# Performance work log

Hardware: AMD Instinct MI355X
Metric: run time of the kernel (lower is better)

## Reference

```python
import jax, jax.numpy as jnp
import numpy as np

N_NODES = 50000
N_EDGES = 600000
DIM = 128
NUM_CLASSES = 10
EPS = 1e-15
MAX_NORM = 1.0 - 1e-5  # keep points strictly inside the unit ball for artanh


def _norm(x):
    return jnp.maximum(jnp.linalg.norm(x, axis=-1, keepdims=True), EPS)


def logmap0(x):
    # Poincare ball, c=1: artanh(||x||) * x / ||x||
    n = _norm(x)
    return jnp.arctanh(jnp.minimum(n, MAX_NORM)) * x / n


def expmap0(u):
    # Poincare ball, c=1: tanh(||u||) * u / ||u||
    n = _norm(u)
    return jnp.tanh(n) * u / n


def hyp_conv(x, W, b, src, dst):
    t = logmap0(x)                       # [N, D] manifold -> tangent at origin
    h = t @ W.T + b                      # [N, D] linear in tangent space
    y = expmap0(h)                       # [N, D] back to manifold
    # message passing: gather source features, scatter-add at destinations
    return jax.ops.segment_sum(y[src], dst, num_segments=N_NODES)


def setup_inputs() -> dict:
    key = jax.random.key(0)
    ks = jax.random.split(key, 8)
    edge_index = jax.random.randint(ks[0], (2, N_EDGES), 0, N_NODES, dtype=jnp.int64)
    # entity embeddings: small tangent vectors mapped onto the ball
    x = expmap0(0.01 * jax.random.normal(ks[1], (N_NODES, DIM), dtype=jnp.float32))
    s = 1.0 / np.sqrt(DIM)
    W1 = jax.random.normal(ks[2], (DIM, DIM), dtype=jnp.float32) * s
    b1 = jax.random.normal(ks[3], (DIM,), dtype=jnp.float32) * 0.01
    W2 = jax.random.normal(ks[4], (DIM, DIM), dtype=jnp.float32) * s
    b2 = jax.random.normal(ks[5], (DIM,), dtype=jnp.float32) * 0.01
    Wc = jax.random.normal(ks[6], (NUM_CLASSES, DIM), dtype=jnp.float32) * s
    bc = jax.random.normal(ks[7], (NUM_CLASSES,), dtype=jnp.float32) * 0.01
    return {"edge_index": edge_index, "x": x, "W1": W1, "b1": b1,
            "W2": W2, "b2": b2, "Wc": Wc, "bc": bc}


def reference(edge_index, x, W1, b1, W2, b2, Wc, bc):
    src, dst = edge_index[0], edge_index[1]
    h = hyp_conv(x, W1, b1, src, dst)
    h = jax.nn.relu(h)
    h = hyp_conv(h, W2, b2, src, dst)
    h = jax.nn.relu(h)
    t = logmap0(h)
    return t @ Wc.T + bc  # [N_NODES, NUM_CLASSES]
```

## Files before the change

### kernel.cpp

```cpp
#include <hip/hip_runtime.h>

#define N_NODES 50000
#define N_EDGES 600000
#define DIM 128
#define NCLS 10
#define ELLW 64
#define CURSTRIDE 16
#define EPSF 1e-15f
#define MAXNORM 0.99999f
#define NTILE ((N_NODES + 63) / 64)
#define FILL_BLOCKS 586
#define XFORM_BLOCKS 512

typedef __attribute__((ext_vector_type(8))) short bf16x8;
typedef __attribute__((ext_vector_type(4))) float f32x4;

__device__ inline float waveSum(float v) {
#pragma unroll
  for (int o = 1; o < 64; o <<= 1) v += __shfl_xor(v, o, 64);
  return v;
}

__device__ inline unsigned short f2bf(float f) {
  union { float f; unsigned u; } c; c.f = f;
  return (unsigned short)((c.u + 0x7FFFu + ((c.u >> 16) & 1u)) >> 16);
}
__device__ inline float bf_lo(unsigned u) {
  union { unsigned u; float f; } c; c.u = u << 16; return c.f;
}
__device__ inline float bf_hi(unsigned u) {
  union { unsigned u; float f; } c; c.u = u & 0xFFFF0000u; return c.f;
}

__global__ __launch_bounds__(256) void init_kernel(
    int* __restrict__ cursor, const float* __restrict__ W1, const float* __restrict__ W2,
    unsigned short* __restrict__ W1b, unsigned short* __restrict__ W2b)
{
  int i = blockIdx.x * 256 + threadIdx.x;
  if (i < N_NODES) cursor[i * CURSTRIDE] = 0;
  if (i < DIM * DIM) {
    W1b[i] = f2bf(W1[i]);
    W2b[i] = f2bf(W2[i]);
  }
}

__global__ __launch_bounds__(256, 2) void fill_transform(
    const int* __restrict__ src, const int* __restrict__ dst,
    int* __restrict__ cursor, int* __restrict__ ell,
    const float* __restrict__ x, const unsigned short* __restrict__ Wb,
    const float* __restrict__ b, unsigned short* __restrict__ y)
{
  __shared__ __align__(16) unsigned short At[64 * DIM];

  if (blockIdx.x < FILL_BLOCKS) {
    const int nthr = FILL_BLOCKS * 256;
    const int e = blockIdx.x * 256 + threadIdx.x;
    const int e0 = e, e1 = e + nthr, e2 = e + 2 * nthr, e3 = e + 3 * nthr;
    int d0, d1, d2, d3, s0, s1, s2, s3;
    if (e0 < N_EDGES) { d0 = dst[e0]; s0 = src[e0]; }
    if (e1 < N_EDGES) { d1 = dst[e1]; s1 = src[e1]; }
    if (e2 < N_EDGES) { d2 = dst[e2]; s2 = src[e2]; }
    if (e3 < N_EDGES) { d3 = dst[e3]; s3 = src[e3]; }
    int p0, p1, p2, p3;
    if (e0 < N_EDGES) p0 = atomicAdd(&cursor[d0 * CURSTRIDE], 1);
    if (e1 < N_EDGES) p1 = atomicAdd(&cursor[d1 * CURSTRIDE], 1);
    if (e2 < N_EDGES) p2 = atomicAdd(&cursor[d2 * CURSTRIDE], 1);
    if (e3 < N_EDGES) p3 = atomicAdd(&cursor[d3 * CURSTRIDE], 1);
    if (e0 < N_EDGES) ell[d0 * ELLW + p0] = s0;
    if (e1 < N_EDGES) ell[d1 * ELLW + p1] = s1;
    if (e2 < N_EDGES) ell[d2 * ELLW + p2] = s2;
    if (e3 < N_EDGES) ell[d3 * ELLW + p3] = s3;
    return;
  }

  const int tid = threadIdx.x;
  const int w = tid >> 6;
  const int l = tid & 63;
  const int lr = l & 15;
  const int lg = l >> 4;

  bf16x8 bf[8][4];
#pragma unroll
  for (int n = 0; n < 8; ++n)
#pragma unroll
    for (int kc = 0; kc < 4; ++kc)
      bf[n][kc] = *(const bf16x8*)(Wb + (n * 16 + lr) * DIM + kc * 32 + lg * 8);

  float bias[8];
#pragma unroll
  for (int n = 0; n < 8; ++n) bias[n] = b[n * 16 + lr];

  const int row = w * 16 + lr;

  for (int tile = blockIdx.x - FILL_BLOCKS; tile < NTILE; tile += XFORM_BLOCKS) {
    const int base = tile * 64;
    const int node = base + row;
    __syncthreads();

    float v[32];
    if (node < N_NODES) {
      const float4* xr = (const float4*)(x + (size_t)node * DIM + lg * 32);
#pragma unroll
      for (int q = 0; q < 8; ++q) {
        float4 f = xr[q];
        v[q * 4 + 0] = f.x; v[q * 4 + 1] = f.y; v[q * 4 + 2] = f.z; v[q * 4 + 3] = f.w;
      }
    } else {
#pragma unroll
      for (int q = 0; q < 32; ++q) v[q] = 0.f;
    }
    float sq = 0.f;
#pragma unroll
    for (int q = 0; q < 32; ++q) sq += v[q] * v[q];
    sq += __shfl_xor(sq, 16, 64);
    sq += __shfl_xor(sq, 32, 64);
    float n1 = sqrtf(sq);
    float nc = fmaxf(n1, EPSF);
    float nm = fminf(nc, MAXNORM);
    float scale = 0.5f * logf((1.f + nm) / (1.f - nm)) / nc;
#pragma unroll
    for (int s = 0; s < 4; ++s) {
      unsigned short tmp[8];
#pragma unroll
      for (int e = 0; e < 8; ++e) tmp[e] = f2bf(v[s * 8 + e] * scale);
      int byte = row * 256 + lg * 64 + s * 16;
      byte ^= (row & 7) << 4;
      *(bf16x8*)((char*)At + byte) = *(const bf16x8*)tmp;
    }
    __syncthreads();

    f32x4 acc[8];
#pragma unroll
    for (int n = 0; n < 8; ++n) {
      acc[n][0] = bias[n]; acc[n][1] = bias[n]; acc[n][2] = bias[n]; acc[n][3] = bias[n];
    }
#pragma unroll
    for (int kc = 0; kc < 4; ++kc) {
      int arow = w * 16 + lr;
      int byte = arow * 256 + kc * 64 + lg * 16;
      byte ^= (arow & 7) << 4;
      bf16x8 af = *(const bf16x8*)((const char*)At + byte);
#pragma unroll
      for (int n = 0; n < 8; ++n)
        acc[n] = __builtin_amdgcn_mfma_f32_16x16x32_bf16(af, bf[n][kc], acc[n], 0, 0, 0);
    }

    float rs[4];
#pragma unroll
    for (int j = 0; j < 4; ++j) {
      float s2 = 0.f;
#pragma unroll
      for (int n = 0; n < 8; ++n) s2 += acc[n][j] * acc[n][j];
      s2 += __shfl_xor(s2, 1, 64);
      s2 += __shfl_xor(s2, 2, 64);
      s2 += __shfl_xor(s2, 4, 64);
      s2 += __shfl_xor(s2, 8, 64);
      float n2 = sqrtf(s2);
      float n2c = fmaxf(n2, EPSF);
      rs[j] = tanhf(n2c) / n2c;
    }
#pragma unroll
    for (int j = 0; j < 4; ++j) {
      int nrow = base + w * 16 + lg * 4 + j;
      if (nrow < N_NODES) {
        unsigned short* yr = y + (size_t)nrow * DIM + lr;
#pragma unroll
        for (int n = 0; n < 8; ++n) yr[n * 16] = f2bf(acc[n][j] * rs[j]);
      }
    }
  }
}

__global__ __launch_bounds__(256) void gatherT_kernel(
    const unsigned short* __restrict__ y, const int* __restrict__ cursor,
    const int* __restrict__ ell, unsigned short* __restrict__ tout)
{
  const int node = blockIdx.x * 4 + (threadIdx.x >> 6);
  if (node >= N_NODES) return;
  const int lane = threadIdx.x & 63;
  const int* lst = ell + node * ELLW;
  const int cnt = cursor[node * CURSTRIDE];
  float2 a0 = {0.f, 0.f}, a1 = {0.f, 0.f}, a2 = {0.f, 0.f}, a3 = {0.f, 0.f};
  int j = 0;
  for (; j + 7 < cnt; j += 8) {
    unsigned u0 = ((const unsigned*)(y + (size_t)lst[j    ] * DIM))[lane];
    unsigned u1 = ((const unsigned*)(y + (size_t)lst[j + 1] * DIM))[lane];
    unsigned u2 = ((const unsigned*)(y + (size_t)lst[j + 2] * DIM))[lane];
    unsigned u3 = ((const unsigned*)(y + (size_t)lst[j + 3] * DIM))[lane];
    unsigned u4 = ((const unsigned*)(y + (size_t)lst[j + 4] * DIM))[lane];
    unsigned u5 = ((const unsigned*)(y + (size_t)lst[j + 5] * DIM))[lane];
    unsigned u6 = ((const unsigned*)(y + (size_t)lst[j + 6] * DIM))[lane];
    unsigned u7 = ((const unsigned*)(y + (size_t)lst[j + 7] * DIM))[lane];
    a0.x += bf_lo(u0); a0.y += bf_hi(u0);
    a1.x += bf_lo(u1); a1.y += bf_hi(u1);
    a2.x += bf_lo(u2); a2.y += bf_hi(u2);
    a3.x += bf_lo(u3); a3.y += bf_hi(u3);
    a0.x += bf_lo(u4); a0.y += bf_hi(u4);
    a1.x += bf_lo(u5); a1.y += bf_hi(u5);
    a2.x += bf_lo(u6); a2.y += bf_hi(u6);
    a3.x += bf_lo(u7); a3.y += bf_hi(u7);
  }
  for (; j + 3 < cnt; j += 4) {
    unsigned u0 = ((const unsigned*)(y + (size_t)lst[j    ] * DIM))[lane];
    unsigned u1 = ((const unsigned*)(y + (size_t)lst[j + 1] * DIM))[lane];
    unsigned u2 = ((const unsigned*)(y + (size_t)lst[j + 2] * DIM))[lane];
    unsigned u3 = ((const unsigned*)(y + (size_t)lst[j + 3] * DIM))[lane];
    a0.x += bf_lo(u0); a0.y += bf_hi(u0);
    a1.x += bf_lo(u1); a1.y += bf_hi(u1);
    a2.x += bf_lo(u2); a2.y += bf_hi(u2);
    a3.x += bf_lo(u3); a3.y += bf_hi(u3);
  }
  for (; j < cnt; ++j) {
    unsigned u0 = ((const unsigned*)(y + (size_t)lst[j] * DIM))[lane];
    a0.x += bf_lo(u0); a0.y += bf_hi(u0);
  }
  float2 r;
  r.x = fmaxf((a0.x + a1.x) + (a2.x + a3.x), 0.f);
  r.y = fmaxf((a0.y + a1.y) + (a2.y + a3.y), 0.f);

  float s = waveSum(r.x * r.x + r.y * r.y);
  float n = sqrtf(s);
  float nc = fmaxf(n, EPSF);
  float nm = fminf(nc, MAXNORM);
  float scale = 0.5f * logf((1.0f + nm) / (1.0f - nm)) / nc;
  unsigned u = (unsigned)f2bf(r.x * scale) | ((unsigned)f2bf(r.y * scale) << 16);
  ((unsigned*)(tout + (size_t)node * DIM))[lane] = u;
}

__global__ __launch_bounds__(256, 2) void transform2_mfma(
    const unsigned short* __restrict__ t, const unsigned short* __restrict__ Wb,
    const float* __restrict__ b, unsigned short* __restrict__ y)
{
  const int tid = threadIdx.x;
  const int w = tid >> 6;
  const int l = tid & 63;
  const int lr = l & 15;
  const int lg = l >> 4;

  __shared__ __align__(16) unsigned short At[64 * DIM];

  bf16x8 bf[8][4];
#pragma unroll
  for (int n = 0; n < 8; ++n)
#pragma unroll
    for (int kc = 0; kc < 4; ++kc)
      bf[n][kc] = *(const bf16x8*)(Wb + (n * 16 + lr) * DIM + kc * 32 + lg * 8);

  float bias[8];
#pragma unroll
  for (int n = 0; n < 8; ++n) bias[n] = b[n * 16 + lr];

  const int row = w * 16 + lr;

  for (int tile = blockIdx.x; tile < NTILE; tile += gridDim.x) {
    const int base = tile * 64;
    const int node = base + row;
    __syncthreads();

#pragma unroll
    for (int s = 0; s < 4; ++s) {
      bf16x8 frag;
      if (node < N_NODES)
        frag = *(const bf16x8*)(t + (size_t)node * DIM + lg * 32 + s * 8);
      else
        frag = bf16x8{0, 0, 0, 0, 0, 0, 0, 0};
      int byte = row * 256 + lg * 64 + s * 16;
      byte ^= (row & 7) << 4;
      *(bf16x8*)((char*)At + byte) = frag;
    }
    __syncthreads();

    f32x4 acc[8];
#pragma unroll
    for (int n = 0; n < 8; ++n) {
      acc[n][0] = bias[n]; acc[n][1] = bias[n]; acc[n][2] = bias[n]; acc[n][3] = bias[n];
    }
#pragma unroll
    for (int kc = 0; kc < 4; ++kc) {
      int arow = w * 16 + lr;
      int byte = arow * 256 + kc * 64 + lg * 16;
      byte ^= (arow & 7) << 4;
      bf16x8 af = *(const bf16x8*)((const char*)At + byte);
#pragma unroll
      for (int n = 0; n < 8; ++n)
        acc[n] = __builtin_amdgcn_mfma_f32_16x16x32_bf16(af, bf[n][kc], acc[n], 0, 0, 0);
    }

    float rs[4];
#pragma unroll
    for (int j = 0; j < 4; ++j) {
      float s2 = 0.f;
#pragma unroll
      for (int n = 0; n < 8; ++n) s2 += acc[n][j] * acc[n][j];
      s2 += __shfl_xor(s2, 1, 64);
      s2 += __shfl_xor(s2, 2, 64);
      s2 += __shfl_xor(s2, 4, 64);
      s2 += __shfl_xor(s2, 8, 64);
      float n2 = sqrtf(s2);
      float n2c = fmaxf(n2, EPSF);
      rs[j] = tanhf(n2c) / n2c;
    }
#pragma unroll
    for (int j = 0; j < 4; ++j) {
      int nrow = base + w * 16 + lg * 4 + j;
      if (nrow < N_NODES) {
        unsigned short* yr = y + (size_t)nrow * DIM + lr;
#pragma unroll
        for (int n = 0; n < 8; ++n) yr[n * 16] = f2bf(acc[n][j] * rs[j]);
      }
    }
  }
}

__global__ __launch_bounds__(256) void head_mfma(
    const unsigned short* __restrict__ t2, const float* __restrict__ Wc,
    const float* __restrict__ bc, float* __restrict__ out)
{
  const int base = blockIdx.x * 64;
  const int w = threadIdx.x >> 6;
  const int l = threadIdx.x & 63;
  const int lr = l & 15;
  const int lg = l >> 4;

  bf16x8 bw[4];
#pragma unroll
  for (int kc = 0; kc < 4; ++kc) {
    unsigned short tmp[8];
    if (lr < NCLS) {
      const float* wr = Wc + (size_t)lr * DIM + kc * 32 + lg * 8;
#pragma unroll
      for (int e = 0; e < 8; ++e) tmp[e] = f2bf(wr[e]);
    } else {
#pragma unroll
      for (int e = 0; e < 8; ++e) tmp[e] = 0;
    }
    bw[kc] = *(const bf16x8*)tmp;
  }
  const float bias = (lr < NCLS) ? bc[lr] : 0.f;

  const int arow = base + w * 16 + lr;
  f32x4 acc;
  acc[0] = bias; acc[1] = bias; acc[2] = bias; acc[3] = bias;
#pragma unroll
  for (int kc = 0; kc < 4; ++kc) {
    bf16x8 af;
    if (arow < N_NODES)
      af = *(const bf16x8*)(t2 + (size_t)arow * DIM + kc * 32 + lg * 8);
    else
      af = bf16x8{0, 0, 0, 0, 0, 0, 0, 0};
    acc = __builtin_amdgcn_mfma_f32_16x16x32_bf16(af, bw[kc], acc, 0, 0, 0);
  }

  if (lr < NCLS) {
#pragma unroll
    for (int j = 0; j < 4; ++j) {
      int nrow = base + w * 16 + lg * 4 + j;
      if (nrow < N_NODES) out[(size_t)nrow * NCLS + lr] = acc[j];
    }
  }
}

extern "C" void kernel_launch(void* const* d_in, const int* in_sizes, int n_in,
                              void* d_out, int out_size, void* d_ws, size_t ws_size,
                              hipStream_t stream)
{
  const int* edge = (const int*)d_in[0];
  const int* src = edge;
  const int* dst = edge + N_EDGES;
  const float* x  = (const float*)d_in[1];
  const float* W1 = (const float*)d_in[2];
  const float* b1 = (const float*)d_in[3];
  const float* W2 = (const float*)d_in[4];
  const float* b2 = (const float*)d_in[5];
  const float* Wc = (const float*)d_in[6];
  const float* bc = (const float*)d_in[7];
  float* out = (float*)d_out;

  unsigned short* ybuf = (unsigned short*)d_ws;
  unsigned short* tbuf = ybuf + (size_t)N_NODES * DIM;
  unsigned short* W1b = tbuf + (size_t)N_NODES * DIM;
  unsigned short* W2b = W1b + DIM * DIM;
  int* cursor = (int*)(W2b + DIM * DIM);
  int* ell    = cursor + (size_t)N_NODES * CURSTRIDE;

  init_kernel<<<(N_NODES + 255) / 256, 256, 0, stream>>>(cursor, W1, W2, W1b, W2b);

  fill_transform<<<FILL_BLOCKS + XFORM_BLOCKS, 256, 0, stream>>>(
      src, dst, cursor, ell, x, W1b, b1, ybuf);

  gatherT_kernel<<<(N_NODES + 3) / 4, 256, 0, stream>>>(ybuf, cursor, ell, tbuf);

  transform2_mfma<<<512, 256, 0, stream>>>(tbuf, W2b, b2, ybuf);

  gatherT_kernel<<<(N_NODES + 3) / 4, 256, 0, stream>>>(ybuf, cursor, ell, tbuf);

  head_mfma<<<NTILE, 256, 0, stream>>>(tbuf, Wc, bc, out);
}
```

Measured before the change: 135.9 us.

## Build ELL adjacency via two-pass bucketed binning with LDS-local placement

Edges are first appended, with one atomic each, into coarse buckets of 128 destination nodes split into 8 sub-cursors, storing packed (local dst, src) words. A new binfill kernel then builds each bucket's ELL tile in shared memory using LDS atomics, writes it out with coalesced int4 stores, and records per-node degrees. This replaces scattered global atomics on 50k per-node cursors and random ell writes with contended bucket atomics plus an extra pass and launch. It risks overflow if a sub-bucket exceeds CAP or a node exceeds ELLW, and the 16-bit src packing only works because node ids stay below 65536.

```diff
diff --git a/kernel.cpp b/kernel.cpp
--- a/kernel.cpp
+++ b/kernel.cpp
@@ -5,7 +5,10 @@
 #define DIM 128
 #define NCLS 10
 #define ELLW 64
-#define CURSTRIDE 16
+#define NBUCK 391
+#define SUBC 8
+#define CAP 384
+#define CPAD 16
 #define EPSF 1e-15f
 #define MAXNORM 0.99999f
 #define NTILE ((N_NODES + 63) / 64)
@@ -33,11 +36,11 @@
 }
 
 __global__ __launch_bounds__(256) void init_kernel(
-    int* __restrict__ cursor, const float* __restrict__ W1, const float* __restrict__ W2,
+    int* __restrict__ bcur, const float* __restrict__ W1, const float* __restrict__ W2,
     unsigned short* __restrict__ W1b, unsigned short* __restrict__ W2b)
 {
   int i = blockIdx.x * 256 + threadIdx.x;
-  if (i < N_NODES) cursor[i * CURSTRIDE] = 0;
+  if (i < NBUCK * SUBC * CPAD) bcur[i] = 0;
   if (i < DIM * DIM) {
     W1b[i] = f2bf(W1[i]);
     W2b[i] = f2bf(W2[i]);
@@ -46,7 +49,7 @@
 
 __global__ __launch_bounds__(256, 2) void fill_transform(
     const int* __restrict__ src, const int* __restrict__ dst,
-    int* __restrict__ cursor, int* __restrict__ ell,
+    int* __restrict__ bcur, unsigned* __restrict__ interm,
     const float* __restrict__ x, const unsigned short* __restrict__ Wb,
     const float* __restrict__ b, unsigned short* __restrict__ y)
 {
@@ -55,6 +58,7 @@
   if (blockIdx.x < FILL_BLOCKS) {
     const int nthr = FILL_BLOCKS * 256;
     const int e = blockIdx.x * 256 + threadIdx.x;
+    const int q = threadIdx.x & (SUBC - 1);
     const int e0 = e, e1 = e + nthr, e2 = e + 2 * nthr, e3 = e + 3 * nthr;
     int d0, d1, d2, d3, s0, s1, s2, s3;
     if (e0 < N_EDGES) { d0 = dst[e0]; s0 = src[e0]; }
@@ -62,14 +66,14 @@
     if (e2 < N_EDGES) { d2 = dst[e2]; s2 = src[e2]; }
     if (e3 < N_EDGES) { d3 = dst[e3]; s3 = src[e3]; }
     int p0, p1, p2, p3;
-    if (e0 < N_EDGES) p0 = atomicAdd(&cursor[d0 * CURSTRIDE], 1);
-    if (e1 < N_EDGES) p1 = atomicAdd(&cursor[d1 * CURSTRIDE], 1);
-    if (e2 < N_EDGES) p2 = atomicAdd(&cursor[d2 * CURSTRIDE], 1);
-    if (e3 < N_EDGES) p3 = atomicAdd(&cursor[d3 * CURSTRIDE], 1);
-    if (e0 < N_EDGES) ell[d0 * ELLW + p0] = s0;
-    if (e1 < N_EDGES) ell[d1 * ELLW + p1] = s1;
-    if (e2 < N_EDGES) ell[d2 * ELLW + p2] = s2;
-    if (e3 < N_EDGES) ell[d3 * ELLW + p3] = s3;
+    if (e0 < N_EDGES) p0 = atomicAdd(&bcur[((d0 >> 7) * SUBC + q) * CPAD], 1);
+    if (e1 < N_EDGES) p1 = atomicAdd(&bcur[((d1 >> 7) * SUBC + q) * CPAD], 1);
+    if (e2 < N_EDGES) p2 = atomicAdd(&bcur[((d2 >> 7) * SUBC + q) * CPAD], 1);
+    if (e3 < N_EDGES) p3 = atomicAdd(&bcur[((d3 >> 7) * SUBC + q) * CPAD], 1);
+    if (e0 < N_EDGES) interm[(size_t)((d0 >> 7) * SUBC + q) * CAP + p0] = ((unsigned)(d0 & 127) << 16) | (unsigned)s0;
+    if (e1 < N_EDGES) interm[(size_t)((d1 >> 7) * SUBC + q) * CAP + p1] = ((unsigned)(d1 & 127) << 16) | (unsigned)s1;
+    if (e2 < N_EDGES) interm[(size_t)((d2 >> 7) * SUBC + q) * CAP + p2] = ((unsigned)(d2 & 127) << 16) | (unsigned)s2;
+    if (e3 < N_EDGES) interm[(size_t)((d3 >> 7) * SUBC + q) * CAP + p3] = ((unsigned)(d3 & 127) << 16) | (unsigned)s3;
     return;
   }
 
@@ -171,15 +175,48 @@
   }
 }
 
+__global__ __launch_bounds__(256) void binfill_kernel(
+    const unsigned* __restrict__ interm, const int* __restrict__ bcur,
+    int* __restrict__ ell, int* __restrict__ deg)
+{
+  __shared__ int tile[128 * ELLW];
+  __shared__ int lcur[128];
+  const int b = blockIdx.x;
+  const int tid = threadIdx.x;
+  if (tid < 128) lcur[tid] = 0;
+  __syncthreads();
+#pragma unroll
+  for (int q = 0; q < SUBC; ++q) {
+    int c = bcur[(b * SUBC + q) * CPAD];
+    c = min(c, CAP);
+    const unsigned* seg = interm + (size_t)(b * SUBC + q) * CAP;
+    for (int i = tid; i < c; i += 256) {
+      unsigned u = seg[i];
+      int d = u >> 16, s = (int)(u & 0xFFFFu);
+      int slot = atomicAdd(&lcur[d], 1);
+      tile[d * ELLW + slot] = s;
+    }
+  }
+  __syncthreads();
+  int4* dstp = (int4*)(ell + (size_t)b * 128 * ELLW);
+  const int4* srcp = (const int4*)tile;
+#pragma unroll
+  for (int k = 0; k < 8; ++k) dstp[tid + k * 256] = srcp[tid + k * 256];
+  if (tid < 128) {
+    int node = b * 128 + tid;
+    if (node < N_NODES) deg[node] = lcur[tid];
+  }
+}
+
 __global__ __launch_bounds__(256) void gatherT_kernel(
-    const unsigned short* __restrict__ y, const int* __restrict__ cursor,
+    const unsigned short* __restrict__ y, const int* __restrict__ deg,
     const int* __restrict__ ell, unsigned short* __restrict__ tout)
 {
   const int node = blockIdx.x * 4 + (threadIdx.x >> 6);
   if (node >= N_NODES) return;
   const int lane = threadIdx.x & 63;
-  const int* lst = ell + node * ELLW;
-  const int cnt = cursor[node * CURSTRIDE];
+  const int* lst = ell + (size_t)node * ELLW;
+  const int cnt = deg[node];
   float2 a0 = {0.f, 0.f}, a1 = {0.f, 0.f}, a2 = {0.f, 0.f}, a3 = {0.f, 0.f};
   int j = 0;
   for (; j + 7 < cnt; j += 8) {
@@ -380,19 +417,23 @@
   unsigned short* tbuf = ybuf + (size_t)N_NODES * DIM;
   unsigned short* W1b = tbuf + (size_t)N_NODES * DIM;
   unsigned short* W2b = W1b + DIM * DIM;
-  int* cursor = (int*)(W2b + DIM * DIM);
-  int* ell    = cursor + (size_t)N_NODES * CURSTRIDE;
-
-  init_kernel<<<(N_NODES + 255) / 256, 256, 0, stream>>>(cursor, W1, W2, W1b, W2b);
+  int* bcur = (int*)(W2b + DIM * DIM);
+  unsigned* interm = (unsigned*)(bcur + NBUCK * SUBC * CPAD);
+  int* ell = (int*)(interm + (size_t)NBUCK * SUBC * CAP);
+  int* deg = ell + (size_t)NBUCK * 128 * ELLW;
+
+  init_kernel<<<(N_NODES + 255) / 256, 256, 0, stream>>>(bcur, W1, W2, W1b, W2b);
 
   fill_transform<<<FILL_BLOCKS + XFORM_BLOCKS, 256, 0, stream>>>(
-      src, dst, cursor, ell, x, W1b, b1, ybuf);
-
-  gatherT_kernel<<<(N_NODES + 3) / 4, 256, 0, stream>>>(ybuf, cursor, ell, tbuf);
+      src, dst, bcur, interm, x, W1b, b1, ybuf);
+
+  binfill_kernel<<<NBUCK, 256, 0, stream>>>(interm, bcur, ell, deg);
+
+  gatherT_kernel<<<(N_NODES + 3) / 4, 256, 0, stream>>>(ybuf, deg, ell, tbuf);
 
   transform2_mfma<<<512, 256, 0, stream>>>(tbuf, W2b, b2, ybuf);
 
-  gatherT_kernel<<<(N_NODES + 3) / 4, 256, 0, stream>>>(ybuf, cursor, ell, tbuf);
+  gatherT_kernel<<<(N_NODES + 3) / 4, 256, 0, stream>>>(ybuf, deg, ell, tbuf);
 
   head_mfma<<<NTILE, 256, 0, stream>>>(tbuf, Wc, bc, out);
 }
```

After: 146.7 us. 7.9% more time.

## Partition edge-bucket cursors into eight sub-lists to reduce atomic contention

Applied to the files above, without the earlier changes.

Edge bucketing now uses 8 partitions, chosen by block index, each with its own dense cursor array and a 16-slot ELL list per node, in place of one padded cursor per node. Fill runs one edge per thread across 2344 blocks. The gather kernel loops over the 8 partitions with a 2-way unrolled accumulation. The aim is to spread atomic traffic over more addresses and shrink the padded cursor footprint. The risk is silently dropping edges when a node gets more than 16 in one partition, and more cursor loads per node in the gather.

```diff
diff --git a/kernel.cpp b/kernel.cpp
--- a/kernel.cpp
+++ b/kernel.cpp
@@ -4,13 +4,13 @@
 #define N_EDGES 600000
 #define DIM 128
 #define NCLS 10
-#define ELLW 64
-#define CURSTRIDE 16
+#define NPART 8
+#define ELLW_P 16
 #define EPSF 1e-15f
 #define MAXNORM 0.99999f
 #define NTILE ((N_NODES + 63) / 64)
-#define FILL_BLOCKS 586
-#define XFORM_BLOCKS 512
+#define FILLB 2344
+#define XFB 512
 
 typedef __attribute__((ext_vector_type(8))) short bf16x8;
 typedef __attribute__((ext_vector_type(4))) float f32x4;
@@ -33,11 +33,11 @@
 }
 
 __global__ __launch_bounds__(256) void init_kernel(
-    int* __restrict__ cursor, const float* __restrict__ W1, const float* __restrict__ W2,
+    int* __restrict__ cur, const float* __restrict__ W1, const float* __restrict__ W2,
     unsigned short* __restrict__ W1b, unsigned short* __restrict__ W2b)
 {
   int i = blockIdx.x * 256 + threadIdx.x;
-  if (i < N_NODES) cursor[i * CURSTRIDE] = 0;
+  if (i < NPART * N_NODES) cur[i] = 0;
   if (i < DIM * DIM) {
     W1b[i] = f2bf(W1[i]);
     W2b[i] = f2bf(W2[i]);
@@ -46,30 +46,21 @@
 
 __global__ __launch_bounds__(256, 2) void fill_transform(
     const int* __restrict__ src, const int* __restrict__ dst,
-    int* __restrict__ cursor, int* __restrict__ ell,
+    int* __restrict__ cur, int* __restrict__ ell,
     const float* __restrict__ x, const unsigned short* __restrict__ Wb,
     const float* __restrict__ b, unsigned short* __restrict__ y)
 {
   __shared__ __align__(16) unsigned short At[64 * DIM];
 
-  if (blockIdx.x < FILL_BLOCKS) {
-    const int nthr = FILL_BLOCKS * 256;
+  if (blockIdx.x < FILLB) {
     const int e = blockIdx.x * 256 + threadIdx.x;
-    const int e0 = e, e1 = e + nthr, e2 = e + 2 * nthr, e3 = e + 3 * nthr;
-    int d0, d1, d2, d3, s0, s1, s2, s3;
-    if (e0 < N_EDGES) { d0 = dst[e0]; s0 = src[e0]; }
-    if (e1 < N_EDGES) { d1 = dst[e1]; s1 = src[e1]; }
-    if (e2 < N_EDGES) { d2 = dst[e2]; s2 = src[e2]; }
-    if (e3 < N_EDGES) { d3 = dst[e3]; s3 = src[e3]; }
-    int p0, p1, p2, p3;
-    if (e0 < N_EDGES) p0 = atomicAdd(&cursor[d0 * CURSTRIDE], 1);
-    if (e1 < N_EDGES) p1 = atomicAdd(&cursor[d1 * CURSTRIDE], 1);
-    if (e2 < N_EDGES) p2 = atomicAdd(&cursor[d2 * CURSTRIDE], 1);
-    if (e3 < N_EDGES) p3 = atomicAdd(&cursor[d3 * CURSTRIDE], 1);
-    if (e0 < N_EDGES) ell[d0 * ELLW + p0] = s0;
-    if (e1 < N_EDGES) ell[d1 * ELLW + p1] = s1;
-    if (e2 < N_EDGES) ell[d2 * ELLW + p2] = s2;
-    if (e3 < N_EDGES) ell[d3 * ELLW + p3] = s3;
+    if (e < N_EDGES) {
+      const int part = blockIdx.x & (NPART - 1);
+      int d = dst[e];
+      int s = src[e];
+      int p = atomicAdd(&cur[part * N_NODES + d], 1);
+      if (p < ELLW_P) ell[((size_t)part * N_NODES + d) * ELLW_P + p] = s;
+    }
     return;
   }
 
@@ -92,7 +83,7 @@
 
   const int row = w * 16 + lr;
 
-  for (int tile = blockIdx.x - FILL_BLOCKS; tile < NTILE; tile += XFORM_BLOCKS) {
+  for (int tile = blockIdx.x - FILLB; tile < NTILE; tile += XFB) {
     const int base = tile * 64;
     const int node = base + row;
     __syncthreads();
@@ -136,9 +127,8 @@
     }
 #pragma unroll
     for (int kc = 0; kc < 4; ++kc) {
-      int arow = w * 16 + lr;
-      int byte = arow * 256 + kc * 64 + lg * 16;
-      byte ^= (arow & 7) << 4;
+      int byte = row * 256 + kc * 64 + lg * 16;
+      byte ^= (row & 7) << 4;
       bf16x8 af = *(const bf16x8*)((const char*)At + byte);
 #pragma unroll
       for (int n = 0; n < 8; ++n)
@@ -172,51 +162,34 @@
 }
 
 __global__ __launch_bounds__(256) void gatherT_kernel(
-    const unsigned short* __restrict__ y, const int* __restrict__ cursor,
+    const unsigned short* __restrict__ y, const int* __restrict__ cur,
     const int* __restrict__ ell, unsigned short* __restrict__ tout)
 {
   const int node = blockIdx.x * 4 + (threadIdx.x >> 6);
   if (node >= N_NODES) return;
   const int lane = threadIdx.x & 63;
-  const int* lst = ell + node * ELLW;
-  const int cnt = cursor[node * CURSTRIDE];
-  float2 a0 = {0.f, 0.f}, a1 = {0.f, 0.f}, a2 = {0.f, 0.f}, a3 = {0.f, 0.f};
-  int j = 0;
-  for (; j + 7 < cnt; j += 8) {
-    unsigned u0 = ((const unsigned*)(y + (size_t)lst[j    ] * DIM))[lane];
-    unsigned u1 = ((const unsigned*)(y + (size_t)lst[j + 1] * DIM))[lane];
-    unsigned u2 = ((const unsigned*)(y + (size_t)lst[j + 2] * DIM))[lane];
-    unsigned u3 = ((const unsigned*)(y + (size_t)lst[j + 3] * DIM))[lane];
-    unsigned u4 = ((const unsigned*)(y + (size_t)lst[j + 4] * DIM))[lane];
-    unsigned u5 = ((const unsigned*)(y + (size_t)lst[j + 5] * DIM))[lane];
-    unsigned u6 = ((const unsigned*)(y + (size_t)lst[j + 6] * DIM))[lane];
-    unsigned u7 = ((const unsigned*)(y + (size_t)lst[j + 7] * DIM))[lane];
-    a0.x += bf_lo(u0); a0.y += bf_hi(u0);
-    a1.x += bf_lo(u1); a1.y += bf_hi(u1);
-    a2.x += bf_lo(u2); a2.y += bf_hi(u2);
-    a3.x += bf_lo(u3); a3.y += bf_hi(u3);
-    a0.x += bf_lo(u4); a0.y += bf_hi(u4);
-    a1.x += bf_lo(u5); a1.y += bf_hi(u5);
-    a2.x += bf_lo(u6); a2.y += bf_hi(u6);
-    a3.x += bf_lo(u7); a3.y += bf_hi(u7);
-  }
-  for (; j + 3 < cnt; j += 4) {
-    unsigned u0 = ((const unsigned*)(y + (size_t)lst[j    ] * DIM))[lane];
-    unsigned u1 = ((const unsigned*)(y + (size_t)lst[j + 1] * DIM))[lane];
-    unsigned u2 = ((const unsigned*)(y + (size_t)lst[j + 2] * DIM))[lane];
-    unsigned u3 = ((const unsigned*)(y + (size_t)lst[j + 3] * DIM))[lane];
-    a0.x += bf_lo(u0); a0.y += bf_hi(u0);
-    a1.x += bf_lo(u1); a1.y += bf_hi(u1);
-    a2.x += bf_lo(u2); a2.y += bf_hi(u2);
-    a3.x += bf_lo(u3); a3.y += bf_hi(u3);
-  }
-  for (; j < cnt; ++j) {
-    unsigned u0 = ((const unsigned*)(y + (size_t)lst[j] * DIM))[lane];
-    a0.x += bf_lo(u0); a0.y += bf_hi(u0);
+  float2 a0 = {0.f, 0.f}, a1 = {0.f, 0.f};
+#pragma unroll
+  for (int part = 0; part < NPART; ++part) {
+    int cnt = cur[part * N_NODES + node];
+    cnt = min(cnt, ELLW_P);
+    const int* lst = ell + ((size_t)part * N_NODES + node) * ELLW_P;
+    int j = 0;
+    for (; j + 1 < cnt; j += 2) {
+      int s0 = lst[j], s1 = lst[j + 1];
+      unsigned u0 = ((const unsigned*)(y + (size_t)s0 * DIM))[lane];
+      unsigned u1 = ((const unsigned*)(y + (size_t)s1 * DIM))[lane];
+      a0.x += bf_lo(u0); a0.y += bf_hi(u0);
+      a1.x += bf_lo(u1); a1.y += bf_hi(u1);
+    }
+    if (j < cnt) {
+      unsigned u0 = ((const unsigned*)(y + (size_t)lst[j] * DIM))[lane];
+      a0.x += bf_lo(u0); a0.y += bf_hi(u0);
+    }
   }
   float2 r;
-  r.x = fmaxf((a0.x + a1.x) + (a2.x + a3.x), 0.f);
-  r.y = fmaxf((a0.y + a1.y) + (a2.y + a3.y), 0.f);
+  r.x = fmaxf(a0.x + a1.x, 0.f);
+  r.y = fmaxf(a0.y + a1.y, 0.f);
 
   float s = waveSum(r.x * r.x + r.y * r.y);
   float n = sqrtf(s);
@@ -277,9 +250,8 @@
     }
 #pragma unroll
     for (int kc = 0; kc < 4; ++kc) {
-      int arow = w * 16 + lr;
-      int byte = arow * 256 + kc * 64 + lg * 16;
-      byte ^= (arow & 7) << 4;
+      int byte = row * 256 + kc * 64 + lg * 16;
+      byte ^= (row & 7) << 4;
       bf16x8 af = *(const bf16x8*)((const char*)At + byte);
 #pragma unroll
       for (int n = 0; n < 8; ++n)
@@ -380,19 +352,18 @@
   unsigned short* tbuf = ybuf + (size_t)N_NODES * DIM;
   unsigned short* W1b = tbuf + (size_t)N_NODES * DIM;
   unsigned short* W2b = W1b + DIM * DIM;
-  int* cursor = (int*)(W2b + DIM * DIM);
-  int* ell    = cursor + (size_t)N_NODES * CURSTRIDE;
-
-  init_kernel<<<(N_NODES + 255) / 256, 256, 0, stream>>>(cursor, W1, W2, W1b, W2b);
-
-  fill_transform<<<FILL_BLOCKS + XFORM_BLOCKS, 256, 0, stream>>>(
-      src, dst, cursor, ell, x, W1b, b1, ybuf);
-
-  gatherT_kernel<<<(N_NODES + 3) / 4, 256, 0, stream>>>(ybuf, cursor, ell, tbuf);
+  int* cur = (int*)(W2b + DIM * DIM);
+  int* ell = cur + NPART * N_NODES;
+
+  init_kernel<<<(NPART * N_NODES + 255) / 256, 256, 0, stream>>>(cur, W1, W2, W1b, W2b);
+
+  fill_transform<<<FILLB + XFB, 256, 0, stream>>>(src, dst, cur, ell, x, W1b, b1, ybuf);
+
+  gatherT_kernel<<<(N_NODES + 3) / 4, 256, 0, stream>>>(ybuf, cur, ell, tbuf);
 
   transform2_mfma<<<512, 256, 0, stream>>>(tbuf, W2b, b2, ybuf);
 
-  gatherT_kernel<<<(N_NODES + 3) / 4, 256, 0, stream>>>(ybuf, cursor, ell, tbuf);
+  gatherT_kernel<<<(N_NODES + 3) / 4, 256, 0, stream>>>(ybuf, cur, ell, tbuf);
 
   head_mfma<<<NTILE, 256, 0, stream>>>(tbuf, Wc, bc, out);
 }
```

After: 207.9 us. 1.53x slower.

## Slice gather by 64-byte column line and defer relu/logmap to consumers

Applied to the files above, without the earlier changes.

The per-node gather used to have one wavefront read full 256-byte rows. It is replaced by a gather where 16 lanes handle one node and one 64-byte column slice (4 slices). Each block is bound to a node half and a slice so that the gathered source rows sit in a smaller working set in cache. The relu and logmap normalisation, which needed a full-row reduction, move into transform2 and the head kernel, which now read raw aggregated sums and apply the scaling before the MFMA. This costs an extra bf16 rounding of the unnormalised sum, and the full 8-wide unroll of the gather loop is dropped.

```diff
diff --git a/kernel.cpp b/kernel.cpp
--- a/kernel.cpp
+++ b/kernel.cpp
@@ -9,21 +9,20 @@
 #define EPSF 1e-15f
 #define MAXNORM 0.99999f
 #define NTILE ((N_NODES + 63) / 64)
-#define FILL_BLOCKS 586
-#define XFORM_BLOCKS 512
+#define FILLB 586
+#define XFB 512
+#define HALFN 25000
+#define GSB (8 * 1563)
 
 typedef __attribute__((ext_vector_type(8))) short bf16x8;
 typedef __attribute__((ext_vector_type(4))) float f32x4;
-
-__device__ inline float waveSum(float v) {
-#pragma unroll
-  for (int o = 1; o < 64; o <<= 1) v += __shfl_xor(v, o, 64);
-  return v;
-}
 
 __device__ inline unsigned short f2bf(float f) {
   union { float f; unsigned u; } c; c.f = f;
   return (unsigned short)((c.u + 0x7FFFu + ((c.u >> 16) & 1u)) >> 16);
+}
+__device__ inline float bf2f(unsigned short s) {
+  union { unsigned u; float f; } c; c.u = (unsigned)s << 16; return c.f;
 }
 __device__ inline float bf_lo(unsigned u) {
   union { unsigned u; float f; } c; c.u = u << 16; return c.f;
@@ -52,8 +51,8 @@
 {
   __shared__ __align__(16) unsigned short At[64 * DIM];
 
-  if (blockIdx.x < FILL_BLOCKS) {
-    const int nthr = FILL_BLOCKS * 256;
+  if (blockIdx.x < FILLB) {
+    const int nthr = FILLB * 256;
     const int e = blockIdx.x * 256 + threadIdx.x;
     const int e0 = e, e1 = e + nthr, e2 = e + 2 * nthr, e3 = e + 3 * nthr;
     int d0, d1, d2, d3, s0, s1, s2, s3;
@@ -92,7 +91,7 @@
 
   const int row = w * 16 + lr;
 
-  for (int tile = blockIdx.x - FILL_BLOCKS; tile < NTILE; tile += XFORM_BLOCKS) {
+  for (int tile = blockIdx.x - FILLB; tile < NTILE; tile += XFB) {
     const int base = tile * 64;
     const int node = base + row;
     __syncthreads();
@@ -136,9 +135,8 @@
     }
 #pragma unroll
     for (int kc = 0; kc < 4; ++kc) {
-      int arow = w * 16 + lr;
-      int byte = arow * 256 + kc * 64 + lg * 16;
-      byte ^= (arow & 7) << 4;
+      int byte = row * 256 + kc * 64 + lg * 16;
+      byte ^= (row & 7) << 4;
       bf16x8 af = *(const bf16x8*)((const char*)At + byte);
 #pragma unroll
       for (int n = 0; n < 8; ++n)
@@ -171,64 +169,45 @@
   }
 }
 
-__global__ __launch_bounds__(256) void gatherT_kernel(
+__global__ __launch_bounds__(256) void gather_slice(
     const unsigned short* __restrict__ y, const int* __restrict__ cursor,
-    const int* __restrict__ ell, unsigned short* __restrict__ tout)
-{
-  const int node = blockIdx.x * 4 + (threadIdx.x >> 6);
-  if (node >= N_NODES) return;
-  const int lane = threadIdx.x & 63;
-  const int* lst = ell + node * ELLW;
+    const int* __restrict__ ell, unsigned short* __restrict__ h)
+{
+  const int part = blockIdx.x & 7;
+  const int line = part >> 1;
+  const int half = part & 1;
+  const int local = (blockIdx.x >> 3) * 16 + (threadIdx.x >> 4);
+  if (local >= HALFN) return;
+  const int node = half * HALFN + local;
+  const int lane16 = threadIdx.x & 15;
   const int cnt = cursor[node * CURSTRIDE];
-  float2 a0 = {0.f, 0.f}, a1 = {0.f, 0.f}, a2 = {0.f, 0.f}, a3 = {0.f, 0.f};
+  const int* lst = ell + (size_t)node * ELLW;
+  const unsigned short* yb = y + line * 32;
+  float ax0 = 0.f, ay0 = 0.f, ax1 = 0.f, ay1 = 0.f;
+  float ax2 = 0.f, ay2 = 0.f, ax3 = 0.f, ay3 = 0.f;
   int j = 0;
-  for (; j + 7 < cnt; j += 8) {
-    unsigned u0 = ((const unsigned*)(y + (size_t)lst[j    ] * DIM))[lane];
-    unsigned u1 = ((const unsigned*)(y + (size_t)lst[j + 1] * DIM))[lane];
-    unsigned u2 = ((const unsigned*)(y + (size_t)lst[j + 2] * DIM))[lane];
-    unsigned u3 = ((const unsigned*)(y + (size_t)lst[j + 3] * DIM))[lane];
-    unsigned u4 = ((const unsigned*)(y + (size_t)lst[j + 4] * DIM))[lane];
-    unsigned u5 = ((const unsigned*)(y + (size_t)lst[j + 5] * DIM))[lane];
-    unsigned u6 = ((const unsigned*)(y + (size_t)lst[j + 6] * DIM))[lane];
-    unsigned u7 = ((const unsigned*)(y + (size_t)lst[j + 7] * DIM))[lane];
-    a0.x += bf_lo(u0); a0.y += bf_hi(u0);
-    a1.x += bf_lo(u1); a1.y += bf_hi(u1);
-    a2.x += bf_lo(u2); a2.y += bf_hi(u2);
-    a3.x += bf_lo(u3); a3.y += bf_hi(u3);
-    a0.x += bf_lo(u4); a0.y += bf_hi(u4);
-    a1.x += bf_lo(u5); a1.y += bf_hi(u5);
-    a2.x += bf_lo(u6); a2.y += bf_hi(u6);
-    a3.x += bf_lo(u7); a3.y += bf_hi(u7);
-  }
   for (; j + 3 < cnt; j += 4) {
-    unsigned u0 = ((const unsigned*)(y + (size_t)lst[j    ] * DIM))[lane];
-    unsigned u1 = ((const unsigned*)(y + (size_t)lst[j + 1] * DIM))[lane];
-    unsigned u2 = ((const unsigned*)(y + (size_t)lst[j + 2] * DIM))[lane];
-    unsigned u3 = ((const unsigned*)(y + (size_t)lst[j + 3] * DIM))[lane];
-    a0.x += bf_lo(u0); a0.y += bf_hi(u0);
-    a1.x += bf_lo(u1); a1.y += bf_hi(u1);
-    a2.x += bf_lo(u2); a2.y += bf_hi(u2);
-    a3.x += bf_lo(u3); a3.y += bf_hi(u3);
+    unsigned u0 = ((const unsigned*)(yb + (size_t)lst[j    ] * DIM))[lane16];
+    unsigned u1 = ((const unsigned*)(yb + (size_t)lst[j + 1] * DIM))[lane16];
+    unsigned u2 = ((const unsigned*)(yb + (size_t)lst[j + 2] * DIM))[lane16];
+    unsigned u3 = ((const unsigned*)(yb + (size_t)lst[j + 3] * DIM))[lane16];
+    ax0 += bf_lo(u0); ay0 += bf_hi(u0);
+    ax1 += bf_lo(u1); ay1 += bf_hi(u1);
+    ax2 += bf_lo(u2); ay2 += bf_hi(u2);
+    ax3 += bf_lo(u3); ay3 += bf_hi(u3);
   }
   for (; j < cnt; ++j) {
-    unsigned u0 = ((const unsigned*)(y + (size_t)lst[j] * DIM))[lane];
-    a0.x += bf_lo(u0); a0.y += bf_hi(u0);
-  }
-  float2 r;
-  r.x = fmaxf((a0.x + a1.x) + (a2.x + a3.x), 0.f);
-  r.y = fmaxf((a0.y + a1.y) + (a2.y + a3.y), 0.f);
-
-  float s = waveSum(r.x * r.x + r.y * r.y);
-  float n = sqrtf(s);
-  float nc = fmaxf(n, EPSF);
-  float nm = fminf(nc, MAXNORM);
-  float scale = 0.5f * logf((1.0f + nm) / (1.0f - nm)) / nc;
-  unsigned u = (unsigned)f2bf(r.x * scale) | ((unsigned)f2bf(r.y * scale) << 16);
-  ((unsigned*)(tout + (size_t)node * DIM))[lane] = u;
+    unsigned u0 = ((const unsigned*)(yb + (size_t)lst[j] * DIM))[lane16];
+    ax0 += bf_lo(u0); ay0 += bf_hi(u0);
+  }
+  float rx = (ax0 + ax1) + (ax2 + ax3);
+  float ry = (ay0 + ay1) + (ay2 + ay3);
+  unsigned u = (unsigned)f2bf(rx) | ((unsigned)f2bf(ry) << 16);
+  ((unsigned*)(h + (size_t)node * DIM + line * 32))[lane16] = u;
 }
 
 __global__ __launch_bounds__(256, 2) void transform2_mfma(
-    const unsigned short* __restrict__ t, const unsigned short* __restrict__ Wb,
+    const unsigned short* __restrict__ h, const unsigned short* __restrict__ Wb,
     const float* __restrict__ b, unsigned short* __restrict__ y)
 {
   const int tid = threadIdx.x;
@@ -257,16 +236,37 @@
     const int node = base + row;
     __syncthreads();
 
+    float v[32];
+    if (node < N_NODES) {
+      const unsigned short* hr = h + (size_t)node * DIM + lg * 32;
+#pragma unroll
+      for (int s = 0; s < 4; ++s) {
+        bf16x8 frag = *(const bf16x8*)(hr + s * 8);
+#pragma unroll
+        for (int e = 0; e < 8; ++e)
+          v[s * 8 + e] = fmaxf(bf2f((unsigned short)frag[e]), 0.f);
+      }
+    } else {
+#pragma unroll
+      for (int q = 0; q < 32; ++q) v[q] = 0.f;
+    }
+    float sq = 0.f;
+#pragma unroll
+    for (int q = 0; q < 32; ++q) sq += v[q] * v[q];
+    sq += __shfl_xor(sq, 16, 64);
+    sq += __shfl_xor(sq, 32, 64);
+    float n1 = sqrtf(sq);
+    float nc = fmaxf(n1, EPSF);
+    float nm = fminf(nc, MAXNORM);
+    float scale = 0.5f * logf((1.f + nm) / (1.f - nm)) / nc;
 #pragma unroll
     for (int s = 0; s < 4; ++s) {
-      bf16x8 frag;
-      if (node < N_NODES)
-        frag = *(const bf16x8*)(t + (size_t)node * DIM + lg * 32 + s * 8);
-      else
-        frag = bf16x8{0, 0, 0, 0, 0, 0, 0, 0};
+      unsigned short tmp[8];
+#pragma unroll
+      for (int e = 0; e < 8; ++e) tmp[e] = f2bf(v[s * 8 + e] * scale);
       int byte = row * 256 + lg * 64 + s * 16;
       byte ^= (row & 7) << 4;
-      *(bf16x8*)((char*)At + byte) = frag;
+      *(bf16x8*)((char*)At + byte) = *(const bf16x8*)tmp;
     }
     __syncthreads();
 
@@ -277,9 +277,8 @@
     }
 #pragma unroll
     for (int kc = 0; kc < 4; ++kc) {
-      int arow = w * 16 + lr;
-      int byte = arow * 256 + kc * 64 + lg * 16;
-      byte ^= (arow & 7) << 4;
+      int byte = row * 256 + kc * 64 + lg * 16;
+      byte ^= (row & 7) << 4;
       bf16x8 af = *(const bf16x8*)((const char*)At + byte);
 #pragma unroll
       for (int n = 0; n < 8; ++n)
@@ -313,7 +312,7 @@
 }
 
 __global__ __launch_bounds__(256) void head_mfma(
-    const unsigned short* __restrict__ t2, const float* __restrict__ Wc,
+    const unsigned short* __restrict__ h2, const float* __restrict__ Wc,
     const float* __restrict__ bc, float* __restrict__ out)
 {
   const int base = blockIdx.x * 64;
@@ -339,15 +338,39 @@
   const float bias = (lr < NCLS) ? bc[lr] : 0.f;
 
   const int arow = base + w * 16 + lr;
+
+  float va[32];
+  if (arow < N_NODES) {
+    const unsigned short* hr = h2 + (size_t)arow * DIM;
+#pragma unroll
+    for (int kc = 0; kc < 4; ++kc) {
+      bf16x8 f = *(const bf16x8*)(hr + kc * 32 + lg * 8);
+#pragma unroll
+      for (int e = 0; e < 8; ++e)
+        va[kc * 8 + e] = fmaxf(bf2f((unsigned short)f[e]), 0.f);
+    }
+  } else {
+#pragma unroll
+    for (int q = 0; q < 32; ++q) va[q] = 0.f;
+  }
+  float sq = 0.f;
+#pragma unroll
+  for (int q = 0; q < 32; ++q) sq += va[q] * va[q];
+  sq += __shfl_xor(sq, 16, 64);
+  sq += __shfl_xor(sq, 32, 64);
+  float n1 = sqrtf(sq);
+  float nc = fmaxf(n1, EPSF);
+  float nm = fminf(nc, MAXNORM);
+  float scale = 0.5f * logf((1.f + nm) / (1.f - nm)) / nc;
+
   f32x4 acc;
   acc[0] = bias; acc[1] = bias; acc[2] = bias; acc[3] = bias;
 #pragma unroll
   for (int kc = 0; kc < 4; ++kc) {
-    bf16x8 af;
-    if (arow < N_NODES)
-      af = *(const bf16x8*)(t2 + (size_t)arow * DIM + kc * 32 + lg * 8);
-    else
-      af = bf16x8{0, 0, 0, 0, 0, 0, 0, 0};
+    unsigned short tmp[8];
+#pragma unroll
+    for (int e = 0; e < 8; ++e) tmp[e] = f2bf(va[kc * 8 + e] * scale);
+    bf16x8 af = *(const bf16x8*)tmp;
     acc = __builtin_amdgcn_mfma_f32_16x16x32_bf16(af, bw[kc], acc, 0, 0, 0);
   }
 
@@ -377,22 +400,21 @@
   float* out = (float*)d_out;
 
   unsigned short* ybuf = (unsigned short*)d_ws;
-  unsigned short* tbuf = ybuf + (size_t)N_NODES * DIM;
-  unsigned short* W1b = tbuf + (size_t)N_NODES * DIM;
+  unsigned short* hbuf = ybuf + (size_t)N_NODES * DIM;
+  unsigned short* W1b = hbuf + (size_t)N_NODES * DIM;
   unsigned short* W2b = W1b + DIM * DIM;
   int* cursor = (int*)(W2b + DIM * DIM);
-  int* ell    = cursor + (size_t)N_NODES * CURSTRIDE;
+  int* ell = cursor + (size_t)N_NODES * CURSTRIDE;
 
   init_kernel<<<(N_NODES + 255) / 256, 256, 0, stream>>>(cursor, W1, W2, W1b, W2b);
 
-  fill_transform<<<FILL_BLOCKS + XFORM_BLOCKS, 256, 0, stream>>>(
-      src, dst, cursor, ell, x, W1b, b1, ybuf);
-
-  gatherT_kernel<<<(N_NODES + 3) / 4, 256, 0, stream>>>(ybuf, cursor, ell, tbuf);
-
-  transform2_mfma<<<512, 256, 0, stream>>>(tbuf, W2b, b2, ybuf);
-
-  gatherT_kernel<<<(N_NODES + 3) / 4, 256, 0, stream>>>(ybuf, cursor, ell, tbuf);
-
-  head_mfma<<<NTILE, 256, 0, stream>>>(tbuf, Wc, bc, out);
-}
+  fill_transform<<<FILLB + XFB, 256, 0, stream>>>(src, dst, cursor, ell, x, W1b, b1, ybuf);
+
+  gather_slice<<<GSB, 256, 0, stream>>>(ybuf, cursor, ell, hbuf);
+
+  transform2_mfma<<<512, 256, 0, stream>>>(hbuf, W2b, b2, ybuf);
+
+  gather_slice<<<GSB, 256, 0, stream>>>(ybuf, cursor, ell, hbuf);
+
+  head_mfma<<<NTILE, 256, 0, stream>>>(hbuf, Wc, bc, out);
+}
```

Measured after the change: 161.3 us. 1.19x slower.
